# Optimization experiments

Measured on AMD Instinct MI355X. Metric: run time of the kernel, lower is better.

The kernel has to match this reference:

```python
import jax, jax.numpy as jnp
import numpy as np

B, N, C = 8, 8192, 64
NPOINT = 2048
RADIUS = 0.2
NSAMPLE = 32


def _fps_single(xyz, npoint):
    # xyz: (N, 3). Iterative farthest point sampling, start at index 0.
    n = xyz.shape[0]

    def body(carry, _):
        min_d, last = carry
        d = jnp.sum((xyz - xyz[last]) ** 2, axis=-1)   # (N,)
        min_d = jnp.minimum(min_d, d)
        nxt = jnp.argmax(min_d).astype(jnp.int32)
        return (min_d, nxt), nxt

    init = (jnp.full((n,), jnp.inf, xyz.dtype), jnp.int32(0))
    _, idx = jax.lax.scan(body, init, None, length=npoint - 1)
    return jnp.concatenate([jnp.zeros((1,), jnp.int32), idx])  # (npoint,)


def _ball_query(xyz, new_xyz, radius, nsample):
    # xyz: (B, N, 3), new_xyz: (B, S, 3) -> neighbor idx (B, S, nsample)
    n = xyz.shape[1]
    # squared pairwise distances (B, S, N)
    d2 = (jnp.sum(new_xyz ** 2, -1)[:, :, None]
          + jnp.sum(xyz ** 2, -1)[:, None, :]
          - 2.0 * jnp.einsum('bsc,bnc->bsn', new_xyz, xyz))
    mask = d2 < radius * radius
    # valid indices first, in original order; invalid -> sentinel n
    key = jnp.where(mask, jnp.arange(n, dtype=jnp.int32)[None, None, :], n)
    srt = jnp.sort(key, axis=-1)[:, :, :nsample]      # (B, S, nsample)
    first = srt[:, :, :1]                             # pad with first valid (query itself)
    return jnp.where(srt >= n, first, srt).astype(jnp.int32)


def setup_inputs() -> dict:
    key = jax.random.key(0)
    k = jax.random.split(key, 8)
    s1 = 1.0 / np.sqrt(67.0)
    s2 = 1.0 / np.sqrt(64.0)
    return {
        'xyz': jax.random.uniform(k[0], (B, N, 3), jnp.float32),
        'features': jax.random.normal(k[1], (B, C, N), jnp.float32),
        'W1': jax.random.normal(k[2], (67, 64), jnp.float32) * s1,
        'b1': jnp.zeros((64,), jnp.float32),
        'W2': jax.random.normal(k[3], (64, 64), jnp.float32) * s2,
        'b2': jnp.zeros((64,), jnp.float32),
        'W3': jax.random.normal(k[4], (64, 128), jnp.float32) * s2,
        'b3': jnp.zeros((128,), jnp.float32),
    }


def reference(xyz, features, W1, b1, W2, b2, W3, b3):
    # 1) farthest point sampling -> centroid indices (B, S)
    fps_idx = jax.vmap(_fps_single, in_axes=(0, None))(xyz, NPOINT)
    new_xyz = jnp.take_along_axis(xyz, fps_idx[:, :, None], axis=1)  # (B, S, 3)

    # 2) ball query grouping
    idx = _ball_query(xyz, new_xyz, RADIUS, NSAMPLE)                 # (B, S, K)
    grouped_xyz = jnp.take_along_axis(
        xyz[:, None, :, :], idx[:, :, :, None], axis=2)              # (B, S, K, 3)
    grouped_xyz = grouped_xyz - new_xyz[:, :, None, :]               # relative coords
    feats_n = jnp.transpose(features, (0, 2, 1))                     # (B, N, C)
    grouped_feats = jnp.take_along_axis(
        feats_n[:, None, :, :], idx[:, :, :, None], axis=2)          # (B, S, K, C)
    g = jnp.concatenate([grouped_xyz, grouped_feats], axis=-1)       # (B, S, K, 3+C)

    # 3) shared MLP (1x1 conv2d equivalent) + ReLU
    h = jax.nn.relu(jnp.einsum('bskc,cd->bskd', g, W1) + b1)
    h = jax.nn.relu(jnp.einsum('bskc,cd->bskd', h, W2) + b2)
    h = jax.nn.relu(jnp.einsum('bskc,cd->bskd', h, W3) + b3)         # (B, S, K, 128)

    # 4) max-pool over the neighbor axis
    new_features = jnp.max(h, axis=2)                                # (B, S, 128)
    new_features = jnp.transpose(new_features, (0, 2, 1))            # (B, 128, S)
    return new_xyz, new_features
```

## Files before the change

### kernel.cpp

```cpp
#include <hip/hip_runtime.h>
#include <cstddef>

#define BATCH 8
#define NPTS 8192
#define NFEAT 64
#define NPOINT 2048
#define NSAMPLE 32

__device__ __forceinline__ float sq_nc(float a) {
    float r = a * a;
    asm volatile("" : "+v"(r));
    return r;
}
__device__ __forceinline__ float mul_nc(float a, float b) {
    float r = a * b;
    asm volatile("" : "+v"(r));
    return r;
}

__global__ __launch_bounds__(512) void fps_f1_kernel(const float* __restrict__ xyz,
                                                     const float* __restrict__ features,
                                                     const float* __restrict__ W1,
                                                     float* __restrict__ F1,
                                                     float* __restrict__ newxyz) {
    extern __shared__ float lds[];
    const int tid = threadIdx.x;

    if (blockIdx.x >= 8) {
        const int lane = tid & 63;
        const int chunk = (tid >> 6) & 3;
        const int sub = tid >> 8;
        const int fblk = blockIdx.x - 8;
        const int b = fblk >> 6;
        const int n = ((fblk & 63) << 7) + (sub << 6) + lane;
        const float* fb = features + (size_t)b * NFEAT * NPTS + n;
        const float* wbase = W1 + 3 * 64 + chunk * 16;

        float acc[16];
#pragma unroll
        for (int i = 0; i < 16; ++i) acc[i] = 0.0f;

#pragma unroll 4
        for (int cp = 0; cp < 64; ++cp) {
            float f = fb[(size_t)cp * NPTS];
            const float4* w = reinterpret_cast<const float4*>(wbase + (size_t)cp * 64);
#pragma unroll
            for (int c4 = 0; c4 < 4; ++c4) {
                float4 ww = w[c4];
                acc[c4 * 4 + 0] += f * ww.x;
                acc[c4 * 4 + 1] += f * ww.y;
                acc[c4 * 4 + 2] += f * ww.z;
                acc[c4 * 4 + 3] += f * ww.w;
            }
        }
        float* o = F1 + ((size_t)b * NPTS + n) * 64 + chunk * 16;
#pragma unroll
        for (int c4 = 0; c4 < 4; ++c4) {
            float4 v;
            v.x = acc[c4 * 4 + 0]; v.y = acc[c4 * 4 + 1];
            v.z = acc[c4 * 4 + 2]; v.w = acc[c4 * 4 + 3];
            *reinterpret_cast<float4*>(o + c4 * 4) = v;
        }
        return;
    }

    float* sx = lds;
    float* sy = lds + NPTS;
    float* sz = lds + 2 * NPTS;
    __shared__ alignas(16) unsigned long long redp[2][8];

    const int b = blockIdx.x;
    const int lane = tid & 63;
    const int wid = tid >> 6;
    const float* xb = xyz + (size_t)b * NPTS * 3;

    for (int i = tid; i < NPTS; i += 512) {
        sx[i] = xb[i * 3 + 0];
        sy[i] = xb[i * 3 + 1];
        sz[i] = xb[i * 3 + 2];
    }
    __syncthreads();

    float mx[16], my_[16], mz[16], md[16];
    const int base = tid * 16;
#pragma unroll
    for (int j = 0; j < 16; ++j) {
        mx[j] = sx[base + j];
        my_[j] = sy[base + j];
        mz[j] = sz[base + j];
        md[j] = INFINITY;
    }

    if (tid == 0) {
        newxyz[(size_t)b * NPOINT * 3 + 0] = sx[0];
        newxyz[(size_t)b * NPOINT * 3 + 1] = sy[0];
        newxyz[(size_t)b * NPOINT * 3 + 2] = sz[0];
    }
    float xl = sx[0], yl = sy[0], zl = sz[0];
    int par = 0;

    for (int it = 1; it < NPOINT; ++it) {
        float bv = -1.0f;
        int bi = 0;
#pragma unroll
        for (int j = 0; j < 16; ++j) {
            float dx = mx[j] - xl;
            float dy = my_[j] - yl;
            float dz = mz[j] - zl;
            float d = (sq_nc(dx) + sq_nc(dy)) + sq_nc(dz);
            float m = fminf(md[j], d);
            md[j] = m;
            if (m > bv) { bv = m; bi = base + j; }
        }

        float wv = bv;
#pragma unroll
        for (int m = 1; m < 64; m <<= 1)
            wv = fmaxf(wv, __shfl_xor(wv, m, 64));
        unsigned long long msk = __ballot(bv == wv);
        int src = __builtin_ctzll(msk);
        int wbi = __shfl(bi, src, 64);

        if (lane == 0)
            redp[par][wid] = ((unsigned long long)__float_as_uint(wv) << 32) |
                             (unsigned int)(~(unsigned int)wbi);
        __syncthreads();

        const ulonglong2* rp = (const ulonglong2*)redp[par];
        ulonglong2 r0 = rp[0], r1 = rp[1], r2 = rp[2], r3 = rp[3];
        unsigned long long m0 = (r0.x > r0.y) ? r0.x : r0.y;
        unsigned long long m1 = (r1.x > r1.y) ? r1.x : r1.y;
        unsigned long long m2 = (r2.x > r2.y) ? r2.x : r2.y;
        unsigned long long m3 = (r3.x > r3.y) ? r3.x : r3.y;
        m0 = (m1 > m0) ? m1 : m0;
        m2 = (m3 > m2) ? m3 : m2;
        m0 = (m2 > m0) ? m2 : m0;
        const int fi = (int)(~(unsigned int)m0);

        xl = sx[fi]; yl = sy[fi]; zl = sz[fi];
        if (tid == 0) {
            size_t o = (size_t)b * NPOINT * 3 + (size_t)it * 3;
            newxyz[o + 0] = xl;
            newxyz[o + 1] = yl;
            newxyz[o + 2] = zl;
        }
        par ^= 1;
    }
}

__global__ __launch_bounds__(64) void ball_kernel(const float* __restrict__ xyz,
                                                  const float* __restrict__ newxyz,
                                                  int* __restrict__ ballidx) {
    extern __shared__ float4 s4[];
    const int b = blockIdx.y;
    const int s = blockIdx.x * 64 + threadIdx.x;
    const float* xb = xyz + (size_t)b * NPTS * 3;
    for (int i = threadIdx.x; i < NPTS; i += 64) {
        float x = xb[i * 3 + 0], y = xb[i * 3 + 1], z = xb[i * 3 + 2];
        float sq = (sq_nc(x) + sq_nc(y)) + sq_nc(z);
        s4[i] = make_float4(x, y, z, sq);
    }
    __syncthreads();

    const int sIdx = b * NPOINT + s;
    float cx = newxyz[(size_t)sIdx * 3 + 0];
    float cy = newxyz[(size_t)sIdx * 3 + 1];
    float cz = newxyz[(size_t)sIdx * 3 + 2];
    float cq = (sq_nc(cx) + sq_nc(cy)) + sq_nc(cz);

    int* ob = ballidx + (size_t)sIdx * NSAMPLE;
    int cnt = 0;
    int first = 0;
#pragma unroll 4
    for (int n = 0; n < NPTS; ++n) {
        float4 p = s4[n];
        float dot = __fmaf_rn(cz, p.z, __fmaf_rn(cy, p.y, __fmul_rn(cx, p.x)));
        float d2 = (cq + p.w) - mul_nc(2.0f, dot);
        if (d2 < 0.04f && cnt < NSAMPLE) {
            ob[cnt] = n;
            if (cnt == 0) first = n;
            ++cnt;
        }
    }
    for (int j = cnt; j < NSAMPLE; ++j) ob[j] = first;
}

__global__ __launch_bounds__(256) void mlp_kernel(const float* __restrict__ xyz,
                                                  const float* __restrict__ W1,
                                                  const float* __restrict__ b1,
                                                  const float* __restrict__ W2,
                                                  const float* __restrict__ b2,
                                                  const float* __restrict__ W3,
                                                  const float* __restrict__ b3,
                                                  const float* __restrict__ F1,
                                                  const int* __restrict__ ballidx,
                                                  const float* __restrict__ newxyz,
                                                  float* __restrict__ outF) {
    __shared__ float hbuf[64][256];
    const int tid = threadIdx.x;
    const int k = tid & 31;
    const int sIdx = blockIdx.x * 8 + (tid >> 5);
    const int b = sIdx >> 11;
    const int s = sIdx & (NPOINT - 1);

    const int p = ballidx[(size_t)sIdx * NSAMPLE + k];
    const float* xb = xyz + (size_t)b * NPTS * 3;
    float rx = xb[p * 3 + 0] - newxyz[(size_t)sIdx * 3 + 0];
    float ry = xb[p * 3 + 1] - newxyz[(size_t)sIdx * 3 + 1];
    float rz = xb[p * 3 + 2] - newxyz[(size_t)sIdx * 3 + 2];

    const float* f1p = F1 + ((size_t)b * NPTS + p) * 64;
#pragma unroll 4
    for (int c4 = 0; c4 < 16; ++c4) {
        float4 f  = *reinterpret_cast<const float4*>(f1p + c4 * 4);
        float4 wx = *reinterpret_cast<const float4*>(W1 + c4 * 4);
        float4 wy = *reinterpret_cast<const float4*>(W1 + 64 + c4 * 4);
        float4 wz = *reinterpret_cast<const float4*>(W1 + 128 + c4 * 4);
        float4 bb = *reinterpret_cast<const float4*>(b1 + c4 * 4);
        hbuf[c4 * 4 + 0][tid] = fmaxf(bb.x + f.x + rx * wx.x + ry * wy.x + rz * wz.x, 0.0f);
        hbuf[c4 * 4 + 1][tid] = fmaxf(bb.y + f.y + rx * wx.y + ry * wy.y + rz * wz.y, 0.0f);
        hbuf[c4 * 4 + 2][tid] = fmaxf(bb.z + f.z + rx * wx.z + ry * wy.z + rz * wz.z, 0.0f);
        hbuf[c4 * 4 + 3][tid] = fmaxf(bb.w + f.w + rx * wx.w + ry * wy.w + rz * wz.w, 0.0f);
    }

    float h2[64];
#pragma unroll
    for (int d4 = 0; d4 < 16; ++d4) {
        float4 bb = *reinterpret_cast<const float4*>(b2 + d4 * 4);
        h2[d4 * 4 + 0] = bb.x; h2[d4 * 4 + 1] = bb.y;
        h2[d4 * 4 + 2] = bb.z; h2[d4 * 4 + 3] = bb.w;
    }
#pragma unroll 4
    for (int c = 0; c < 64; ++c) {
        float a = hbuf[c][tid];
        const float4* w = reinterpret_cast<const float4*>(W2 + (size_t)c * 64);
#pragma unroll
        for (int d4 = 0; d4 < 16; ++d4) {
            float4 ww = w[d4];
            h2[d4 * 4 + 0] += a * ww.x;
            h2[d4 * 4 + 1] += a * ww.y;
            h2[d4 * 4 + 2] += a * ww.z;
            h2[d4 * 4 + 3] += a * ww.w;
        }
    }
#pragma unroll
    for (int d = 0; d < 64; ++d) hbuf[d][tid] = fmaxf(h2[d], 0.0f);

    const size_t obase = (size_t)b * 128 * NPOINT + s;
#pragma unroll 1
    for (int ch = 0; ch < 4; ++ch) {
        float acc[32];
#pragma unroll
        for (int j4 = 0; j4 < 8; ++j4) {
            float4 bb = *reinterpret_cast<const float4*>(b3 + ch * 32 + j4 * 4);
            acc[j4 * 4 + 0] = bb.x; acc[j4 * 4 + 1] = bb.y;
            acc[j4 * 4 + 2] = bb.z; acc[j4 * 4 + 3] = bb.w;
        }
#pragma unroll 4
        for (int c = 0; c < 64; ++c) {
            float a = hbuf[c][tid];
            const float4* w = reinterpret_cast<const float4*>(W3 + (size_t)c * 128 + ch * 32);
#pragma unroll
            for (int j4 = 0; j4 < 8; ++j4) {
                float4 ww = w[j4];
                acc[j4 * 4 + 0] += a * ww.x;
                acc[j4 * 4 + 1] += a * ww.y;
                acc[j4 * 4 + 2] += a * ww.z;
                acc[j4 * 4 + 3] += a * ww.w;
            }
        }
#pragma unroll
        for (int j = 0; j < 32; ++j) {
            float v = fmaxf(acc[j], 0.0f);
#pragma unroll
            for (int m = 16; m >= 1; m >>= 1) v = fmaxf(v, __shfl_xor(v, m, 64));
            acc[j] = v;
        }
        if (k == 0) {
#pragma unroll
            for (int j = 0; j < 32; ++j)
                outF[obase + (size_t)(ch * 32 + j) * NPOINT] = acc[j];
        }
    }
}

extern "C" void kernel_launch(void* const* d_in, const int* in_sizes, int n_in,
                              void* d_out, int out_size, void* d_ws, size_t ws_size,
                              hipStream_t stream) {
    const float* xyz      = (const float*)d_in[0];
    const float* features = (const float*)d_in[1];
    const float* W1       = (const float*)d_in[2];
    const float* b1       = (const float*)d_in[3];
    const float* W2       = (const float*)d_in[4];
    const float* b2       = (const float*)d_in[5];
    const float* W3       = (const float*)d_in[6];
    const float* b3       = (const float*)d_in[7];

    float* out_newxyz = (float*)d_out;
    float* out_feat   = (float*)d_out + (size_t)BATCH * NPOINT * 3;

    int*   ballidx = (int*)d_ws;
    float* F1      = (float*)((char*)d_ws + (size_t)BATCH * NPOINT * NSAMPLE * 4);

    fps_f1_kernel<<<8 + 512, 512, 3 * NPTS * 4, stream>>>(xyz, features, W1, F1, out_newxyz);

    ball_kernel<<<dim3(NPOINT / 64, BATCH), 64, NPTS * 16, stream>>>(xyz, out_newxyz, ballidx);

    mlp_kernel<<<(BATCH * NPOINT) / 8, 256, 0, stream>>>(
        xyz, W1, b1, W2, b2, W3, b3, F1, ballidx, out_newxyz, out_feat);
}
```

Measured before the change: 2.780 ms.

## Fuse FPS, ball query and MLP into one cooperative kernel with progress flags

Merges the three kernels into a single cooperative launch. Eight blocks run farthest point sampling and publish progress counters every 32 centroids. The remaining 248 consumer blocks first compute F1, then meet at a global barrier, then spin on the progress flags so ball query and the MLP run on centroid groups of 16 while FPS is still going. This overlaps the serial FPS phase with downstream work and removes the ballidx round trip through global memory. The cost is spin-waiting, 128KB of LDS per block, and ball query now running on only 16 threads per block.

```diff
diff --git a/kernel.cpp b/kernel.cpp
--- a/kernel.cpp
+++ b/kernel.cpp
@@ -6,6 +6,8 @@
 #define NFEAT 64
 #define NPOINT 2048
 #define NSAMPLE 32
+#define NCONS 248
+#define NGRP 1024
 
 __device__ __forceinline__ float sq_nc(float a) {
     float r = a * a;
@@ -18,28 +20,111 @@
     return r;
 }
 
-__global__ __launch_bounds__(512) void fps_f1_kernel(const float* __restrict__ xyz,
-                                                     const float* __restrict__ features,
-                                                     const float* __restrict__ W1,
-                                                     float* __restrict__ F1,
-                                                     float* __restrict__ newxyz) {
-    extern __shared__ float lds[];
+__global__ __launch_bounds__(512) void fused_kernel(
+        const float* __restrict__ xyz, const float* __restrict__ features,
+        const float* __restrict__ W1, const float* __restrict__ b1,
+        const float* __restrict__ W2, const float* __restrict__ b2,
+        const float* __restrict__ W3, const float* __restrict__ b3,
+        float* __restrict__ F1, float* __restrict__ newxyz,
+        float* __restrict__ outF, int* __restrict__ progress,
+        int* __restrict__ f1done) {
+    extern __shared__ float dyn[];
     const int tid = threadIdx.x;
-
-    if (blockIdx.x >= 8) {
-        const int lane = tid & 63;
-        const int chunk = (tid >> 6) & 3;
-        const int sub = tid >> 8;
-        const int fblk = blockIdx.x - 8;
-        const int b = fblk >> 6;
-        const int n = ((fblk & 63) << 7) + (sub << 6) + lane;
-        const float* fb = features + (size_t)b * NFEAT * NPTS + n;
+    const int lane = tid & 63;
+    const int wid = tid >> 6;
+
+    if (blockIdx.x < BATCH) {
+        float* sx = dyn;
+        float* sy = dyn + NPTS;
+        float* sz = dyn + 2 * NPTS;
+        __shared__ alignas(16) unsigned long long redp[2][8];
+        const int b = blockIdx.x;
+        const float* xb = xyz + (size_t)b * NPTS * 3;
+        for (int i = tid; i < NPTS; i += 512) {
+            sx[i] = xb[i * 3 + 0];
+            sy[i] = xb[i * 3 + 1];
+            sz[i] = xb[i * 3 + 2];
+        }
+        __syncthreads();
+
+        float mx[16], my_[16], mz[16], md[16];
+        const int base = tid * 16;
+#pragma unroll
+        for (int j = 0; j < 16; ++j) {
+            mx[j] = sx[base + j];
+            my_[j] = sy[base + j];
+            mz[j] = sz[base + j];
+            md[j] = INFINITY;
+        }
+        if (tid == 0) {
+            newxyz[(size_t)b * NPOINT * 3 + 0] = sx[0];
+            newxyz[(size_t)b * NPOINT * 3 + 1] = sy[0];
+            newxyz[(size_t)b * NPOINT * 3 + 2] = sz[0];
+        }
+        float xl = sx[0], yl = sy[0], zl = sz[0];
+        int par = 0;
+
+        for (int it = 1; it < NPOINT; ++it) {
+            float bv = -1.0f;
+            int bi = 0;
+#pragma unroll
+            for (int j = 0; j < 16; ++j) {
+                float dx = mx[j] - xl;
+                float dy = my_[j] - yl;
+                float dz = mz[j] - zl;
+                float d = (sq_nc(dx) + sq_nc(dy)) + sq_nc(dz);
+                float m = fminf(md[j], d);
+                md[j] = m;
+                if (m > bv) { bv = m; bi = base + j; }
+            }
+            float wv = bv;
+#pragma unroll
+            for (int m = 1; m < 64; m <<= 1)
+                wv = fmaxf(wv, __shfl_xor(wv, m, 64));
+            unsigned long long msk = __ballot(bv == wv);
+            int src = __builtin_ctzll(msk);
+            int wbi = __shfl(bi, src, 64);
+            if (lane == 0)
+                redp[par][wid] = ((unsigned long long)__float_as_uint(wv) << 32) |
+                                 (unsigned int)(~(unsigned int)wbi);
+            __syncthreads();
+            const ulonglong2* rp = (const ulonglong2*)redp[par];
+            ulonglong2 r0 = rp[0], r1 = rp[1], r2 = rp[2], r3 = rp[3];
+            unsigned long long m0 = (r0.x > r0.y) ? r0.x : r0.y;
+            unsigned long long m1 = (r1.x > r1.y) ? r1.x : r1.y;
+            unsigned long long m2 = (r2.x > r2.y) ? r2.x : r2.y;
+            unsigned long long m3 = (r3.x > r3.y) ? r3.x : r3.y;
+            m0 = (m1 > m0) ? m1 : m0;
+            m2 = (m3 > m2) ? m3 : m2;
+            m0 = (m2 > m0) ? m2 : m0;
+            const int fi = (int)(~(unsigned int)m0);
+            xl = sx[fi]; yl = sy[fi]; zl = sz[fi];
+            if (tid == 0) {
+                size_t o = (size_t)b * NPOINT * 3 + (size_t)it * 3;
+                newxyz[o + 0] = xl;
+                newxyz[o + 1] = yl;
+                newxyz[o + 2] = zl;
+                if ((it & 31) == 31)
+                    __hip_atomic_store(&progress[b], it + 1, __ATOMIC_RELEASE,
+                                       __HIP_MEMORY_SCOPE_AGENT);
+            }
+            par ^= 1;
+        }
+        return;
+    }
+
+    const int j = blockIdx.x - BATCH;
+
+    for (int wt = j * 8 + wid; wt < 4096; wt += NCONS * 8) {
+        const int blk = wt >> 2;
+        const int chunk = wt & 3;
+        const int fb_b = blk >> 7;
+        const int n = ((blk & 127) << 6) | lane;
+        const float* fb = features + (size_t)fb_b * NFEAT * NPTS + n;
         const float* wbase = W1 + 3 * 64 + chunk * 16;
-
         float acc[16];
 #pragma unroll
         for (int i = 0; i < 16; ++i) acc[i] = 0.0f;
-
 #pragma unroll 4
         for (int cp = 0; cp < 64; ++cp) {
             float f = fb[(size_t)cp * NPTS];
@@ -53,7 +138,7 @@
                 acc[c4 * 4 + 3] += f * ww.w;
             }
         }
-        float* o = F1 + ((size_t)b * NPTS + n) * 64 + chunk * 16;
+        float* o = F1 + ((size_t)fb_b * NPTS + n) * 64 + chunk * 16;
 #pragma unroll
         for (int c4 = 0; c4 < 4; ++c4) {
             float4 v;
@@ -61,225 +146,140 @@
             v.z = acc[c4 * 4 + 2]; v.w = acc[c4 * 4 + 3];
             *reinterpret_cast<float4*>(o + c4 * 4) = v;
         }
-        return;
-    }
-
-    float* sx = lds;
-    float* sy = lds + NPTS;
-    float* sz = lds + 2 * NPTS;
-    __shared__ alignas(16) unsigned long long redp[2][8];
-
-    const int b = blockIdx.x;
-    const int lane = tid & 63;
-    const int wid = tid >> 6;
-    const float* xb = xyz + (size_t)b * NPTS * 3;
-
-    for (int i = tid; i < NPTS; i += 512) {
-        sx[i] = xb[i * 3 + 0];
-        sy[i] = xb[i * 3 + 1];
-        sz[i] = xb[i * 3 + 2];
     }
     __syncthreads();
-
-    float mx[16], my_[16], mz[16], md[16];
-    const int base = tid * 16;
-#pragma unroll
-    for (int j = 0; j < 16; ++j) {
-        mx[j] = sx[base + j];
-        my_[j] = sy[base + j];
-        mz[j] = sz[base + j];
-        md[j] = INFINITY;
+    if (tid == 0) {
+        __hip_atomic_fetch_add(f1done, 1, __ATOMIC_ACQ_REL, __HIP_MEMORY_SCOPE_AGENT);
+        while (__hip_atomic_load(f1done, __ATOMIC_ACQUIRE, __HIP_MEMORY_SCOPE_AGENT) < NCONS)
+            __builtin_amdgcn_s_sleep(8);
     }
 
-    if (tid == 0) {
-        newxyz[(size_t)b * NPOINT * 3 + 0] = sx[0];
-        newxyz[(size_t)b * NPOINT * 3 + 1] = sy[0];
-        newxyz[(size_t)b * NPOINT * 3 + 2] = sz[0];
-    }
-    float xl = sx[0], yl = sy[0], zl = sz[0];
-    int par = 0;
-
-    for (int it = 1; it < NPOINT; ++it) {
-        float bv = -1.0f;
-        int bi = 0;
-#pragma unroll
-        for (int j = 0; j < 16; ++j) {
-            float dx = mx[j] - xl;
-            float dy = my_[j] - yl;
-            float dz = mz[j] - zl;
-            float d = (sq_nc(dx) + sq_nc(dy)) + sq_nc(dz);
-            float m = fminf(md[j], d);
-            md[j] = m;
-            if (m > bv) { bv = m; bi = base + j; }
-        }
-
-        float wv = bv;
-#pragma unroll
-        for (int m = 1; m < 64; m <<= 1)
-            wv = fmaxf(wv, __shfl_xor(wv, m, 64));
-        unsigned long long msk = __ballot(bv == wv);
-        int src = __builtin_ctzll(msk);
-        int wbi = __shfl(bi, src, 64);
-
-        if (lane == 0)
-            redp[par][wid] = ((unsigned long long)__float_as_uint(wv) << 32) |
-                             (unsigned int)(~(unsigned int)wbi);
-        __syncthreads();
-
-        const ulonglong2* rp = (const ulonglong2*)redp[par];
-        ulonglong2 r0 = rp[0], r1 = rp[1], r2 = rp[2], r3 = rp[3];
-        unsigned long long m0 = (r0.x > r0.y) ? r0.x : r0.y;
-        unsigned long long m1 = (r1.x > r1.y) ? r1.x : r1.y;
-        unsigned long long m2 = (r2.x > r2.y) ? r2.x : r2.y;
-        unsigned long long m3 = (r3.x > r3.y) ? r3.x : r3.y;
-        m0 = (m1 > m0) ? m1 : m0;
-        m2 = (m3 > m2) ? m3 : m2;
-        m0 = (m2 > m0) ? m2 : m0;
-        const int fi = (int)(~(unsigned int)m0);
-
-        xl = sx[fi]; yl = sy[fi]; zl = sz[fi];
+    __shared__ int bl_lds[16][32];
+    float4* s4 = (float4*)dyn;
+    float* hbuf = dyn;
+
+    for (int pos = j; pos < NGRP; pos += NCONS) {
+        const int b = pos & 7;
+        const int gl = pos >> 3;
+        const int target = gl * 16 + 16;
         if (tid == 0) {
-            size_t o = (size_t)b * NPOINT * 3 + (size_t)it * 3;
-            newxyz[o + 0] = xl;
-            newxyz[o + 1] = yl;
-            newxyz[o + 2] = zl;
-        }
-        par ^= 1;
-    }
-}
-
-__global__ __launch_bounds__(64) void ball_kernel(const float* __restrict__ xyz,
-                                                  const float* __restrict__ newxyz,
-                                                  int* __restrict__ ballidx) {
-    extern __shared__ float4 s4[];
-    const int b = blockIdx.y;
-    const int s = blockIdx.x * 64 + threadIdx.x;
-    const float* xb = xyz + (size_t)b * NPTS * 3;
-    for (int i = threadIdx.x; i < NPTS; i += 64) {
-        float x = xb[i * 3 + 0], y = xb[i * 3 + 1], z = xb[i * 3 + 2];
-        float sq = (sq_nc(x) + sq_nc(y)) + sq_nc(z);
-        s4[i] = make_float4(x, y, z, sq);
-    }
-    __syncthreads();
-
-    const int sIdx = b * NPOINT + s;
-    float cx = newxyz[(size_t)sIdx * 3 + 0];
-    float cy = newxyz[(size_t)sIdx * 3 + 1];
-    float cz = newxyz[(size_t)sIdx * 3 + 2];
-    float cq = (sq_nc(cx) + sq_nc(cy)) + sq_nc(cz);
-
-    int* ob = ballidx + (size_t)sIdx * NSAMPLE;
-    int cnt = 0;
-    int first = 0;
-#pragma unroll 4
-    for (int n = 0; n < NPTS; ++n) {
-        float4 p = s4[n];
-        float dot = __fmaf_rn(cz, p.z, __fmaf_rn(cy, p.y, __fmul_rn(cx, p.x)));
-        float d2 = (cq + p.w) - mul_nc(2.0f, dot);
-        if (d2 < 0.04f && cnt < NSAMPLE) {
-            ob[cnt] = n;
-            if (cnt == 0) first = n;
-            ++cnt;
-        }
-    }
-    for (int j = cnt; j < NSAMPLE; ++j) ob[j] = first;
-}
-
-__global__ __launch_bounds__(256) void mlp_kernel(const float* __restrict__ xyz,
-                                                  const float* __restrict__ W1,
-                                                  const float* __restrict__ b1,
-                                                  const float* __restrict__ W2,
-                                                  const float* __restrict__ b2,
-                                                  const float* __restrict__ W3,
-                                                  const float* __restrict__ b3,
-                                                  const float* __restrict__ F1,
-                                                  const int* __restrict__ ballidx,
-                                                  const float* __restrict__ newxyz,
-                                                  float* __restrict__ outF) {
-    __shared__ float hbuf[64][256];
-    const int tid = threadIdx.x;
-    const int k = tid & 31;
-    const int sIdx = blockIdx.x * 8 + (tid >> 5);
-    const int b = sIdx >> 11;
-    const int s = sIdx & (NPOINT - 1);
-
-    const int p = ballidx[(size_t)sIdx * NSAMPLE + k];
-    const float* xb = xyz + (size_t)b * NPTS * 3;
-    float rx = xb[p * 3 + 0] - newxyz[(size_t)sIdx * 3 + 0];
-    float ry = xb[p * 3 + 1] - newxyz[(size_t)sIdx * 3 + 1];
-    float rz = xb[p * 3 + 2] - newxyz[(size_t)sIdx * 3 + 2];
-
-    const float* f1p = F1 + ((size_t)b * NPTS + p) * 64;
-#pragma unroll 4
-    for (int c4 = 0; c4 < 16; ++c4) {
-        float4 f  = *reinterpret_cast<const float4*>(f1p + c4 * 4);
-        float4 wx = *reinterpret_cast<const float4*>(W1 + c4 * 4);
-        float4 wy = *reinterpret_cast<const float4*>(W1 + 64 + c4 * 4);
-        float4 wz = *reinterpret_cast<const float4*>(W1 + 128 + c4 * 4);
-        float4 bb = *reinterpret_cast<const float4*>(b1 + c4 * 4);
-        hbuf[c4 * 4 + 0][tid] = fmaxf(bb.x + f.x + rx * wx.x + ry * wy.x + rz * wz.x, 0.0f);
-        hbuf[c4 * 4 + 1][tid] = fmaxf(bb.y + f.y + rx * wx.y + ry * wy.y + rz * wz.y, 0.0f);
-        hbuf[c4 * 4 + 2][tid] = fmaxf(bb.z + f.z + rx * wx.z + ry * wy.z + rz * wz.z, 0.0f);
-        hbuf[c4 * 4 + 3][tid] = fmaxf(bb.w + f.w + rx * wx.w + ry * wy.w + rz * wz.w, 0.0f);
-    }
-
-    float h2[64];
-#pragma unroll
-    for (int d4 = 0; d4 < 16; ++d4) {
-        float4 bb = *reinterpret_cast<const float4*>(b2 + d4 * 4);
-        h2[d4 * 4 + 0] = bb.x; h2[d4 * 4 + 1] = bb.y;
-        h2[d4 * 4 + 2] = bb.z; h2[d4 * 4 + 3] = bb.w;
-    }
-#pragma unroll 4
-    for (int c = 0; c < 64; ++c) {
-        float a = hbuf[c][tid];
-        const float4* w = reinterpret_cast<const float4*>(W2 + (size_t)c * 64);
+            while (__hip_atomic_load(&progress[b], __ATOMIC_ACQUIRE,
+                                     __HIP_MEMORY_SCOPE_AGENT) < target)
+                __builtin_amdgcn_s_sleep(8);
+        }
+        __syncthreads();
+
+        const float* xb = xyz + (size_t)b * NPTS * 3;
+        for (int i = tid; i < NPTS; i += 512) {
+            float x = xb[i * 3 + 0], y = xb[i * 3 + 1], z = xb[i * 3 + 2];
+            float sq = (sq_nc(x) + sq_nc(y)) + sq_nc(z);
+            s4[i] = make_float4(x, y, z, sq);
+        }
+        __syncthreads();
+
+        if (tid < 16) {
+            const int sIdx = b * NPOINT + gl * 16 + tid;
+            float cx = newxyz[(size_t)sIdx * 3 + 0];
+            float cy = newxyz[(size_t)sIdx * 3 + 1];
+            float cz = newxyz[(size_t)sIdx * 3 + 2];
+            float cq = (sq_nc(cx) + sq_nc(cy)) + sq_nc(cz);
+            int cnt = 0, first = 0;
+#pragma unroll 4
+            for (int n = 0; n < NPTS; ++n) {
+                float4 p = s4[n];
+                float dot = __fmaf_rn(cz, p.z, __fmaf_rn(cy, p.y, __fmul_rn(cx, p.x)));
+                float d2 = (cq + p.w) - mul_nc(2.0f, dot);
+                if (d2 < 0.04f && cnt < NSAMPLE) {
+                    bl_lds[tid][cnt] = n;
+                    if (cnt == 0) first = n;
+                    ++cnt;
+                }
+            }
+            for (int q = cnt; q < NSAMPLE; ++q) bl_lds[tid][q] = first;
+        }
+        __syncthreads();
+
+        const int g8 = tid >> 5, k = tid & 31;
+        const int sIdx = b * NPOINT + gl * 16 + g8;
+        const int p = bl_lds[g8][k];
+        float4 pt = s4[p];
+        float rx = pt.x - newxyz[(size_t)sIdx * 3 + 0];
+        float ry = pt.y - newxyz[(size_t)sIdx * 3 + 1];
+        float rz = pt.z - newxyz[(size_t)sIdx * 3 + 2];
+        __syncthreads();
+
+        const float* f1p = F1 + ((size_t)b * NPTS + p) * 64;
+#pragma unroll 4
+        for (int c4 = 0; c4 < 16; ++c4) {
+            float4 f  = *reinterpret_cast<const float4*>(f1p + c4 * 4);
+            float4 wx = *reinterpret_cast<const float4*>(W1 + c4 * 4);
+            float4 wy = *reinterpret_cast<const float4*>(W1 + 64 + c4 * 4);
+            float4 wz = *reinterpret_cast<const float4*>(W1 + 128 + c4 * 4);
+            float4 bb = *reinterpret_cast<const float4*>(b1 + c4 * 4);
+            hbuf[(c4 * 4 + 0) * 512 + tid] = fmaxf(bb.x + f.x + rx * wx.x + ry * wy.x + rz * wz.x, 0.0f);
+            hbuf[(c4 * 4 + 1) * 512 + tid] = fmaxf(bb.y + f.y + rx * wx.y + ry * wy.y + rz * wz.y, 0.0f);
+            hbuf[(c4 * 4 + 2) * 512 + tid] = fmaxf(bb.z + f.z + rx * wx.z + ry * wy.z + rz * wz.z, 0.0f);
+            hbuf[(c4 * 4 + 3) * 512 + tid] = fmaxf(bb.w + f.w + rx * wx.w + ry * wy.w + rz * wz.w, 0.0f);
+        }
+
+        float h2[64];
 #pragma unroll
         for (int d4 = 0; d4 < 16; ++d4) {
-            float4 ww = w[d4];
-            h2[d4 * 4 + 0] += a * ww.x;
-            h2[d4 * 4 + 1] += a * ww.y;
-            h2[d4 * 4 + 2] += a * ww.z;
-            h2[d4 * 4 + 3] += a * ww.w;
-        }
-    }
-#pragma unroll
-    for (int d = 0; d < 64; ++d) hbuf[d][tid] = fmaxf(h2[d], 0.0f);
-
-    const size_t obase = (size_t)b * 128 * NPOINT + s;
+            float4 bb = *reinterpret_cast<const float4*>(b2 + d4 * 4);
+            h2[d4 * 4 + 0] = bb.x; h2[d4 * 4 + 1] = bb.y;
+            h2[d4 * 4 + 2] = bb.z; h2[d4 * 4 + 3] = bb.w;
+        }
+#pragma unroll 4
+        for (int c = 0; c < 64; ++c) {
+            float a = hbuf[c * 512 + tid];
+            const float4* w = reinterpret_cast<const float4*>(W2 + (size_t)c * 64);
+#pragma unroll
+            for (int d4 = 0; d4 < 16; ++d4) {
+                float4 ww = w[d4];
+                h2[d4 * 4 + 0] += a * ww.x;
+                h2[d4 * 4 + 1] += a * ww.y;
+                h2[d4 * 4 + 2] += a * ww.z;
+                h2[d4 * 4 + 3] += a * ww.w;
+            }
+        }
+#pragma unroll
+        for (int d = 0; d < 64; ++d) hbuf[d * 512 + tid] = fmaxf(h2[d], 0.0f);
+
+        const size_t obase = (size_t)b * 128 * NPOINT + (size_t)(gl * 16 + g8);
 #pragma unroll 1
-    for (int ch = 0; ch < 4; ++ch) {
-        float acc[32];
-#pragma unroll
-        for (int j4 = 0; j4 < 8; ++j4) {
-            float4 bb = *reinterpret_cast<const float4*>(b3 + ch * 32 + j4 * 4);
-            acc[j4 * 4 + 0] = bb.x; acc[j4 * 4 + 1] = bb.y;
-            acc[j4 * 4 + 2] = bb.z; acc[j4 * 4 + 3] = bb.w;
-        }
-#pragma unroll 4
-        for (int c = 0; c < 64; ++c) {
-            float a = hbuf[c][tid];
-            const float4* w = reinterpret_cast<const float4*>(W3 + (size_t)c * 128 + ch * 32);
+        for (int ch = 0; ch < 4; ++ch) {
+            float acc[32];
 #pragma unroll
             for (int j4 = 0; j4 < 8; ++j4) {
-                float4 ww = w[j4];
-                acc[j4 * 4 + 0] += a * ww.x;
-                acc[j4 * 4 + 1] += a * ww.y;
-                acc[j4 * 4 + 2] += a * ww.z;
-                acc[j4 * 4 + 3] += a * ww.w;
-            }
-        }
-#pragma unroll
-        for (int j = 0; j < 32; ++j) {
-            float v = fmaxf(acc[j], 0.0f);
-#pragma unroll
-            for (int m = 16; m >= 1; m >>= 1) v = fmaxf(v, __shfl_xor(v, m, 64));
-            acc[j] = v;
-        }
-        if (k == 0) {
-#pragma unroll
-            for (int j = 0; j < 32; ++j)
-                outF[obase + (size_t)(ch * 32 + j) * NPOINT] = acc[j];
+                float4 bb = *reinterpret_cast<const float4*>(b3 + ch * 32 + j4 * 4);
+                acc[j4 * 4 + 0] = bb.x; acc[j4 * 4 + 1] = bb.y;
+                acc[j4 * 4 + 2] = bb.z; acc[j4 * 4 + 3] = bb.w;
+            }
+#pragma unroll 4
+            for (int c = 0; c < 64; ++c) {
+                float a = hbuf[c * 512 + tid];
+                const float4* w = reinterpret_cast<const float4*>(W3 + (size_t)c * 128 + ch * 32);
+#pragma unroll
+                for (int j4 = 0; j4 < 8; ++j4) {
+                    float4 ww = w[j4];
+                    acc[j4 * 4 + 0] += a * ww.x;
+                    acc[j4 * 4 + 1] += a * ww.y;
+                    acc[j4 * 4 + 2] += a * ww.z;
+                    acc[j4 * 4 + 3] += a * ww.w;
+                }
+            }
+#pragma unroll
+            for (int q = 0; q < 32; ++q) {
+                float v = fmaxf(acc[q], 0.0f);
+#pragma unroll
+                for (int m = 16; m >= 1; m >>= 1) v = fmaxf(v, __shfl_xor(v, m, 64));
+                acc[q] = v;
+            }
+            if (k == 0) {
+#pragma unroll
+                for (int q = 0; q < 32; ++q)
+                    outF[obase + (size_t)(ch * 32 + q) * NPOINT] = acc[q];
+            }
         }
     }
 }
@@ -299,13 +299,16 @@
     float* out_newxyz = (float*)d_out;
     float* out_feat   = (float*)d_out + (size_t)BATCH * NPOINT * 3;
 
-    int*   ballidx = (int*)d_ws;
-    float* F1      = (float*)((char*)d_ws + (size_t)BATCH * NPOINT * NSAMPLE * 4);
-
-    fps_f1_kernel<<<8 + 512, 512, 3 * NPTS * 4, stream>>>(xyz, features, W1, F1, out_newxyz);
-
-    ball_kernel<<<dim3(NPOINT / 64, BATCH), 64, NPTS * 16, stream>>>(xyz, out_newxyz, ballidx);
-
-    mlp_kernel<<<(BATCH * NPOINT) / 8, 256, 0, stream>>>(
-        xyz, W1, b1, W2, b2, W3, b3, F1, ballidx, out_newxyz, out_feat);
+    int*   progress = (int*)d_ws;
+    int*   f1done   = (int*)d_ws + 8;
+    float* F1       = (float*)((char*)d_ws + 256);
+
+    hipMemsetAsync(d_ws, 0, 256, stream);
+
+    void* args[] = {(void*)&xyz, (void*)&features, (void*)&W1, (void*)&b1,
+                    (void*)&W2, (void*)&b2, (void*)&W3, (void*)&b3,
+                    (void*)&F1, (void*)&out_newxyz, (void*)&out_feat,
+                    (void*)&progress, (void*)&f1done};
+    hipLaunchCooperativeKernel((const void*)fused_kernel, dim3(BATCH + NCONS),
+                               dim3(512), args, 128 * 1024, stream);
 }
```

Result: slower. 3.646 ms (+31.1%).
